# Kernel tuning notes

Hardware: AMD Instinct MI355X
Metric: run time of the kernel (lower is better)

The kernel has to match this reference:

```python
import jax, jax.numpy as jnp
import numpy as np

N_NODES = 100000
N_EDGES = 1600000
D_IN = 128
D_OUT = 128


def setup_inputs() -> dict:
    key = jax.random.key(0)
    k1, k2, k3 = jax.random.split(key, 3)
    input_matrix = jax.random.normal(k1, (N_NODES, D_IN), dtype=jnp.float32)
    adjacency_coo_matrix = jax.random.randint(k2, (2, N_EDGES), 0, N_NODES, dtype=jnp.int64)
    # xavier-uniform-like init for the projection weights
    limit = float(np.sqrt(6.0 / (D_IN + D_OUT)))
    W = jax.random.uniform(k3, (D_IN, D_OUT), minval=-limit, maxval=limit, dtype=jnp.float32)
    return {"input_matrix": input_matrix, "adjacency_coo_matrix": adjacency_coo_matrix, "W": W}


def reference(input_matrix, adjacency_coo_matrix, W):
    N = input_matrix.shape[0]
    # add self edges (i -> i) for every node
    self_idx = jnp.arange(N, dtype=adjacency_coo_matrix.dtype)
    src = jnp.concatenate([adjacency_coo_matrix[0], self_idx])  # segment ids (rows of output)
    nbr = jnp.concatenate([adjacency_coo_matrix[1], self_idx])  # gather indices
    # gather neighbor features: [E+N, d_in]
    neighbors = input_matrix[nbr]
    # scatter-mean over destination nodes
    summed = jax.ops.segment_sum(neighbors, src, num_segments=N)
    counts = jax.ops.segment_sum(jnp.ones((src.shape[0],), dtype=input_matrix.dtype), src, num_segments=N)
    mean = summed / counts[:, None]  # counts >= 1 thanks to self edges
    # linear projection
    return mean @ W
```

## Files before the change

kernel.cpp:

```cpp
#include <hip/hip_runtime.h>
#include <stdint.h>

#define DIM 128
#define SB 256

typedef unsigned short u16;
typedef unsigned int u32;
typedef __attribute__((ext_vector_type(8))) short short8;
typedef __attribute__((ext_vector_type(4))) float floatx4;
typedef __attribute__((ext_vector_type(4))) float nt_f32x4;
typedef __attribute__((ext_vector_type(4))) int i32x4;

__device__ __forceinline__ u16 f2bf(float f) {
    u32 u = __float_as_uint(f);
    if ((u & 0x7fffffffu) > 0x7f800000u) return (u16)0x7fc0;
    return (u16)((u + 0x7fffu + ((u >> 16) & 1u)) >> 16);
}

__global__ void __launch_bounds__(256) k_wprep(const float* __restrict__ W,
                                               u16* __restrict__ Wbf,
                                               u16* __restrict__ Yzero,
                                               int* __restrict__ cursor, int N) {
    int g = blockIdx.x * 256 + threadIdx.x;
    if (g < DIM * DIM) {
        int n = g >> 7, k = g & 127;
        Wbf[g] = f2bf(W[k * DIM + n]);
    }
    if (g < N) cursor[g] = 0;
    if (blockIdx.x == 0 && threadIdx.x < 32)
        ((ushort4*)Yzero)[threadIdx.x] = make_ushort4(0, 0, 0, 0);
}

__global__ void __launch_bounds__(512) k_fused(const float4* __restrict__ X4,
                                               const u16* __restrict__ Wbf,
                                               u16* __restrict__ Ybf,
                                               const int* __restrict__ adj,
                                               int* __restrict__ cursor,
                                               int* __restrict__ slots,
                                               int E, int N, int cap, int G, int T) {
    __shared__ __align__(16) u16 wt[DIM * 136];
    int b = blockIdx.x;
    long a0 = ((long)b * G) / T;
    long a1 = ((long)(b + 1) * G) / T;
    if (a1 > a0) {
        int gb = (int)a0;
        int t = threadIdx.x;
        for (int i = t; i < DIM * 16; i += 512) {
            int row = i >> 4, c8 = i & 15;
            *(short8*)&wt[row * 136 + c8 * 8] = *(const short8*)&Wbf[row * 128 + c8 * 8];
        }
        __syncthreads();
        int w = t >> 6, l = t & 63;
        int q = l >> 4, c = l & 15;
        int row0 = (gb * 8 + w) * 16;
        size_t mr = (size_t)min(row0 + c, N - 1) * 32;
        const nt_f32x4* Xnt = (const nt_f32x4*)X4;
        nt_f32x4 u[8];
        #pragma unroll
        for (int kt = 0; kt < 4; ++kt) {
            u[2 * kt]     = __builtin_nontemporal_load(&Xnt[mr + kt * 8 + q * 2]);
            u[2 * kt + 1] = __builtin_nontemporal_load(&Xnt[mr + kt * 8 + q * 2 + 1]);
        }
        floatx4 acc[8] = {};
        #pragma unroll
        for (int kt = 0; kt < 4; ++kt) {
            short8 a;
            nt_f32x4 u0 = u[2 * kt], u1 = u[2 * kt + 1];
            a[0] = (short)f2bf(u0.x); a[1] = (short)f2bf(u0.y);
            a[2] = (short)f2bf(u0.z); a[3] = (short)f2bf(u0.w);
            a[4] = (short)f2bf(u1.x); a[5] = (short)f2bf(u1.y);
            a[6] = (short)f2bf(u1.z); a[7] = (short)f2bf(u1.w);
            #pragma unroll
            for (int nt = 0; nt < 8; ++nt) {
                short8 bb = *(const short8*)&wt[(nt * 16 + c) * 136 + kt * 32 + q * 8];
                acc[nt] = __builtin_amdgcn_mfma_f32_16x16x32_bf16(a, bb, acc[nt], 0, 0, 0);
            }
        }
        #pragma unroll
        for (int r = 0; r < 4; ++r) {
            int orow = row0 + q * 4 + r;
            if (orow < N) {
                u16* yrow = Ybf + (size_t)orow * DIM;
                #pragma unroll
                for (int nt = 0; nt < 8; ++nt)
                    __builtin_nontemporal_store(f2bf(acc[nt][r]), &yrow[nt * 16 + c]);
            }
        }
    } else {
        int sid = b - (int)a1;
        int r = sid & 7;
        int sub = sid >> 3;
        int lo = N / 8 * r + min(r, N % 8);
        int hi = lo + N / 8 + (r < N % 8 ? 1 : 0);
        const i32x4* v4 = (const i32x4*)adj;
        int npair = E >> 3;
        int p = sub * 512 + threadIdx.x;
        if (p < npair) {
            i32x4 s0 = __builtin_nontemporal_load(&v4[2 * p]);
            i32x4 s1 = __builtin_nontemporal_load(&v4[2 * p + 1]);
            int e0 = p * 8;
            int nb[8];
            #pragma unroll
            for (int k = 0; k < 8; ++k)
                nb[k] = __builtin_nontemporal_load(&adj[E + e0 + k]);
            int ds[8] = {s0.x, s0.y, s0.z, s0.w, s1.x, s1.y, s1.z, s1.w};
            int cc[8];
            #pragma unroll
            for (int k = 0; k < 8; ++k) {
                bool hit = (ds[k] >= lo) & (ds[k] < hi);
                cc[k] = hit ? atomicAdd(&cursor[ds[k]], 1) : cap;
            }
            #pragma unroll
            for (int k = 0; k < 8; ++k) {
                if (cc[k] < cap)
                    slots[(size_t)ds[k] * cap + cc[k]] =
                        ((unsigned)nb[k] < (unsigned)N) ? nb[k] : 0;
            }
        }
        if (sub == 0) {
            int tail = E & 7;
            if (threadIdx.x < tail) {
                int e = (E & ~7) + threadIdx.x;
                int d = adj[e];
                if (d >= lo && d < hi) {
                    int nbv = adj[E + e];
                    int c = atomicAdd(&cursor[d], 1);
                    if (c < cap)
                        slots[(size_t)d * cap + c] =
                            ((unsigned)nbv < (unsigned)N) ? nbv : 0;
                }
            }
        }
    }
}

__device__ __forceinline__ void agg_core(const uint4* __restrict__ Yb4,
                                         const int* __restrict__ lst, int deg,
                                         int wid, int grp, int sl, int N,
                                         float4* __restrict__ out4) {
    float acc[8];
    {
        int id0 = (grp == 0) ? wid : N;
        uint4 v = Yb4[(size_t)id0 * 16 + sl];
        u32 c0[4] = {v.x, v.y, v.z, v.w};
        #pragma unroll
        for (int k2 = 0; k2 < 4; ++k2) {
            acc[2 * k2]     = __uint_as_float(c0[k2] << 16);
            acc[2 * k2 + 1] = __uint_as_float(c0[k2] & 0xffff0000u);
        }
    }
    for (int base = 0; base < deg; base += 32) {
        int id[8];
        #pragma unroll
        for (int qi = 0; qi < 8; ++qi) {
            int ee = base + qi * 4 + grp;
            int t = __builtin_nontemporal_load(&lst[ee]);
            id[qi] = (ee < deg) ? t : N;
        }
        uint4 v[8];
        #pragma unroll
        for (int qi = 0; qi < 8; ++qi)
            v[qi] = Yb4[(size_t)id[qi] * 16 + sl];
        #pragma unroll
        for (int qi = 0; qi < 8; ++qi) {
            u32 c0[4] = {v[qi].x, v[qi].y, v[qi].z, v[qi].w};
            #pragma unroll
            for (int k2 = 0; k2 < 4; ++k2) {
                acc[2 * k2]     += __uint_as_float(c0[k2] << 16);
                acc[2 * k2 + 1] += __uint_as_float(c0[k2] & 0xffff0000u);
            }
        }
    }
    #pragma unroll
    for (int j = 0; j < 8; ++j) {
        acc[j] += __shfl_xor(acc[j], 16);
        acc[j] += __shfl_xor(acc[j], 32);
    }
    float inv = 1.0f / (float)(deg + 1);
    if (grp < 2) {
        nt_f32x4 o;
        o.x = acc[grp * 4 + 0] * inv; o.y = acc[grp * 4 + 1] * inv;
        o.z = acc[grp * 4 + 2] * inv; o.w = acc[grp * 4 + 3] * inv;
        __builtin_nontemporal_store(o, (nt_f32x4*)&out4[(size_t)wid * 32 + sl * 2 + grp]);
    }
}

__global__ void __launch_bounds__(256) k_agg_cap(const uint4* __restrict__ Yb4,
                                                 const int* __restrict__ cnt,
                                                 const int* __restrict__ slots,
                                                 float4* __restrict__ out4, int N, int cap) {
    int wid = (blockIdx.x * 256 + threadIdx.x) >> 6;
    int lane = threadIdx.x & 63;
    if (wid >= N) return;
    int deg = min(cnt[wid], cap);
    agg_core(Yb4, slots + (size_t)wid * cap, deg, wid, lane >> 4, lane & 15, N, out4);
}

__global__ void __launch_bounds__(256) k_agg_off(const uint4* __restrict__ Yb4,
                                                 const int* __restrict__ offsets,
                                                 const int* __restrict__ sorted_nbr,
                                                 float4* __restrict__ out4, int N) {
    int wid = (blockIdx.x * 256 + threadIdx.x) >> 6;
    int lane = threadIdx.x & 63;
    if (wid >= N) return;
    int beg = offsets[wid], end = offsets[wid + 1];
    agg_core(Yb4, sorted_nbr + beg, end - beg, wid, lane >> 4, lane & 15, N, out4);
}

__global__ void __launch_bounds__(256) k_hist(const int* __restrict__ adj,
                                              int* __restrict__ counts, int E, int N) {
    int r = blockIdx.x & 7;
    int sub = blockIdx.x >> 3;
    int nsub = gridDim.x >> 3;
    int lo = N / 8 * r + min(r, N % 8);
    int hi = lo + N / 8 + (r < N % 8 ? 1 : 0);
    for (int e = sub * 256 + threadIdx.x; e < E; e += nsub * 256) {
        int d = adj[e];
        if (d >= lo && d < hi) atomicAdd(&counts[d], 1);
    }
}

__global__ void __launch_bounds__(SB) k_bsum(const int* __restrict__ counts,
                                             int* __restrict__ partials, int N) {
    __shared__ int lds[SB];
    int t = threadIdx.x;
    int i = blockIdx.x * SB + t;
    lds[t] = (i < N) ? counts[i] : 0;
    __syncthreads();
    for (int off = SB / 2; off > 0; off >>= 1) {
        if (t < off) lds[t] += lds[t + off];
        __syncthreads();
    }
    if (t == 0) partials[blockIdx.x] = lds[0];
}

__global__ void __launch_bounds__(1024) k_pscan(int* __restrict__ partials,
                                                int* __restrict__ offsets, int nb, int N) {
    __shared__ int lds[1024];
    int t = threadIdx.x;
    int v0 = (t < nb) ? partials[t] : 0;
    lds[t] = v0;
    __syncthreads();
    for (int off = 1; off < 1024; off <<= 1) {
        int v = (t >= off) ? lds[t - off] : 0;
        __syncthreads();
        lds[t] += v;
        __syncthreads();
    }
    if (t < nb) partials[t] = lds[t] - v0;
    if (t == 1023) offsets[N] = lds[1023];
}

__global__ void __launch_bounds__(SB) k_scan_final(const int* __restrict__ counts_in,
                                                   const int* __restrict__ partials,
                                                   int* __restrict__ offsets,
                                                   int* __restrict__ cursor, int N) {
    __shared__ int lds[SB];
    int t = threadIdx.x;
    int i = blockIdx.x * SB + t;
    int c = (i < N) ? counts_in[i] : 0;
    lds[t] = c;
    __syncthreads();
    for (int off = 1; off < SB; off <<= 1) {
        int v = (t >= off) ? lds[t - off] : 0;
        __syncthreads();
        lds[t] += v;
        __syncthreads();
    }
    int excl = lds[t] - c + partials[blockIdx.x];
    if (i < N) {
        offsets[i] = excl;
        cursor[i] = excl;
    }
}

__global__ void __launch_bounds__(256) k_reorder(const int* __restrict__ adj,
                                                 int* __restrict__ cursor,
                                                 int* __restrict__ sorted_nbr, int E, int N) {
    int r = blockIdx.x & 7;
    int sub = blockIdx.x >> 3;
    int nsub = gridDim.x >> 3;
    int lo = N / 8 * r + min(r, N % 8);
    int hi = lo + N / 8 + (r < N % 8 ? 1 : 0);
    for (int e = sub * 256 + threadIdx.x; e < E; e += nsub * 256) {
        int d = adj[e];
        if (d < lo || d >= hi) continue;
        int nb = adj[E + e];
        int pos = atomicAdd(&cursor[d], 1);
        sorted_nbr[pos] = ((unsigned)nb < (unsigned)N) ? nb : 0;
    }
}

__global__ void __launch_bounds__(512) k_gemm_y(const float4* __restrict__ X4,
                                                const u16* __restrict__ Wbf,
                                                u16* __restrict__ Ybf, int N) {
    __shared__ __align__(16) u16 wt[DIM * 136];
    int t = threadIdx.x;
    for (int i = t; i < DIM * 16; i += 512) {
        int row = i >> 4, c8 = i & 15;
        *(short8*)&wt[row * 136 + c8 * 8] = *(const short8*)&Wbf[row * 128 + c8 * 8];
    }
    __syncthreads();
    int w = t >> 6, l = t & 63;
    int q = l >> 4, c = l & 15;
    int row0 = (blockIdx.x * 8 + w) * 16;
    size_t mr = (size_t)min(row0 + c, N - 1) * 32;
    float4 u[8];
    #pragma unroll
    for (int kt = 0; kt < 4; ++kt) {
        u[2 * kt]     = X4[mr + kt * 8 + q * 2];
        u[2 * kt + 1] = X4[mr + kt * 8 + q * 2 + 1];
    }
    floatx4 acc[8] = {};
    #pragma unroll
    for (int kt = 0; kt < 4; ++kt) {
        short8 a;
        float4 u0 = u[2 * kt], u1 = u[2 * kt + 1];
        a[0] = (short)f2bf(u0.x); a[1] = (short)f2bf(u0.y);
        a[2] = (short)f2bf(u0.z); a[3] = (short)f2bf(u0.w);
        a[4] = (short)f2bf(u1.x); a[5] = (short)f2bf(u1.y);
        a[6] = (short)f2bf(u1.z); a[7] = (short)f2bf(u1.w);
        #pragma unroll
        for (int nt = 0; nt < 8; ++nt) {
            short8 bb = *(const short8*)&wt[(nt * 16 + c) * 136 + kt * 32 + q * 8];
            acc[nt] = __builtin_amdgcn_mfma_f32_16x16x32_bf16(a, bb, acc[nt], 0, 0, 0);
        }
    }
    #pragma unroll
    for (int r = 0; r < 4; ++r) {
        int orow = row0 + q * 4 + r;
        if (orow < N) {
            u16* yrow = Ybf + (size_t)orow * DIM;
            #pragma unroll
            for (int nt = 0; nt < 8; ++nt)
                yrow[nt * 16 + c] = f2bf(acc[nt][r]);
        }
    }
}

extern "C" void kernel_launch(void* const* d_in, const int* in_sizes, int n_in,
                              void* d_out, int out_size, void* d_ws, size_t ws_size,
                              hipStream_t stream) {
    int N = in_sizes[0] / DIM;
    int E = in_sizes[1] / 2;
    const float* X = (const float*)d_in[0];
    const int* adj = (const int*)d_in[1];
    const float* W = (const float*)d_in[2];
    float* out = (float*)d_out;

    int G = (N + 127) / 128;
    int npair = E >> 3;
    int S = 8 * ((npair + 511) / 512);
    int T = G + S;

    int wprep_blocks = (N + 255) / 256;

    size_t cur_b  = (size_t)N * 4;
    size_t y_b    = ((size_t)N + 1) * DIM * 2;
    size_t wbf_b  = (size_t)DIM * DIM * 2;

    int cap = 0;
    if (ws_size >= cur_b + (size_t)N * 64 * 4 + y_b + wbf_b) cap = 64;
    else if (ws_size >= cur_b + (size_t)N * 48 * 4 + y_b + wbf_b) cap = 48;

    if (cap) {
        int* cursor = (int*)d_ws;
        int* slots  = cursor + N;
        u16* Ybf    = (u16*)(slots + (size_t)N * cap);
        u16* Wbf    = Ybf + ((size_t)N + 1) * DIM;

        k_wprep<<<wprep_blocks, 256, 0, stream>>>(W, Wbf, Ybf + (size_t)N * DIM, cursor, N);
        k_fused<<<T, 512, 0, stream>>>((const float4*)X, Wbf, Ybf, adj, cursor, slots,
                                       E, N, cap, G, T);
        k_agg_cap<<<(N + 3) / 4, 256, 0, stream>>>((const uint4*)Ybf, cursor, slots,
                                                   (float4*)out, N, cap);
    } else {
        int nb = (N + SB - 1) / SB;
        int* cursor     = (int*)d_ws;
        int* offsets    = cursor + N;
        int* sorted_nbr = offsets + (N + 1);
        int* partials   = sorted_nbr + E;
        u16* Ybf        = (u16*)(partials + 512);
        u16* Wbf        = Ybf + ((size_t)N + 1) * DIM;

        k_wprep<<<wprep_blocks, 256, 0, stream>>>(W, Wbf, Ybf + (size_t)N * DIM, cursor, N);
        k_gemm_y<<<G, 512, 0, stream>>>((const float4*)X, Wbf, Ybf, N);
        k_hist<<<1024, 256, 0, stream>>>(adj, cursor, E, N);
        k_bsum<<<nb, SB, 0, stream>>>(cursor, partials, N);
        k_pscan<<<1, 1024, 0, stream>>>(partials, offsets, nb, N);
        k_scan_final<<<nb, SB, 0, stream>>>(cursor, partials, offsets, cursor, N);
        k_reorder<<<1024, 256, 0, stream>>>(adj, cursor, sorted_nbr, E, N);
        k_agg_off<<<(N + 3) / 4, 256, 0, stream>>>((const uint4*)Ybf, offsets, sorted_nbr,
                                                   (float4*)out, N);
    }
}
```

Before: 249.9 us.

## Map fused GEMM and bucket work per XCD and drop nontemporal hints

Block indices are now split by b&7 so each of the eight interleaved block groups (matching the round-robin XCD dispatch on MI355X) handles its own GEMM row tiles and its own destination-range bucket fill. This keeps each slot-range's atomics and writes, and its share of Y tiles, within one XCD's L2. Nontemporal loads and stores are also replaced with ordinary accesses so Y and the adjacency data can stay in cache for the later aggregation. The risk is less even load balance and extra cache pressure from the streamed X reads.

```diff
diff --git a/kernel.cpp b/kernel.cpp
--- a/kernel.cpp
+++ b/kernel.cpp
@@ -9,7 +9,6 @@
 typedef __attribute__((ext_vector_type(8))) short short8;
 typedef __attribute__((ext_vector_type(4))) float floatx4;
 typedef __attribute__((ext_vector_type(4))) float nt_f32x4;
-typedef __attribute__((ext_vector_type(4))) int i32x4;
 
 __device__ __forceinline__ u16 f2bf(float f) {
     u32 u = __float_as_uint(f);
@@ -37,13 +36,20 @@
                                                const int* __restrict__ adj,
                                                int* __restrict__ cursor,
                                                int* __restrict__ slots,
-                                               int E, int N, int cap, int G, int T) {
+                                               int E, int N, int cap, int G) {
     __shared__ __align__(16) u16 wt[DIM * 136];
     int b = blockIdx.x;
-    long a0 = ((long)b * G) / T;
-    long a1 = ((long)(b + 1) * G) / T;
+    int x = b & 7;
+    int u = b >> 3;
+    int npair = E >> 3;
+    int Sx = (npair + 511) / 512;
+    int Gx = (G + 7 - x) / 8;
+    int Ux = Gx + Sx;
+    if (u >= Ux) return;
+    long a0 = ((long)u * Gx) / Ux;
+    long a1 = ((long)(u + 1) * Gx) / Ux;
     if (a1 > a0) {
-        int gb = (int)a0;
+        int gb = (int)a0 * 8 + x;
         int t = threadIdx.x;
         for (int i = t; i < DIM * 16; i += 512) {
             int row = i >> 4, c8 = i & 15;
@@ -54,18 +60,17 @@
         int q = l >> 4, c = l & 15;
         int row0 = (gb * 8 + w) * 16;
         size_t mr = (size_t)min(row0 + c, N - 1) * 32;
-        const nt_f32x4* Xnt = (const nt_f32x4*)X4;
-        nt_f32x4 u[8];
+        float4 uv[8];
         #pragma unroll
         for (int kt = 0; kt < 4; ++kt) {
-            u[2 * kt]     = __builtin_nontemporal_load(&Xnt[mr + kt * 8 + q * 2]);
-            u[2 * kt + 1] = __builtin_nontemporal_load(&Xnt[mr + kt * 8 + q * 2 + 1]);
+            uv[2 * kt]     = X4[mr + kt * 8 + q * 2];
+            uv[2 * kt + 1] = X4[mr + kt * 8 + q * 2 + 1];
         }
         floatx4 acc[8] = {};
         #pragma unroll
         for (int kt = 0; kt < 4; ++kt) {
             short8 a;
-            nt_f32x4 u0 = u[2 * kt], u1 = u[2 * kt + 1];
+            float4 u0 = uv[2 * kt], u1 = uv[2 * kt + 1];
             a[0] = (short)f2bf(u0.x); a[1] = (short)f2bf(u0.y);
             a[2] = (short)f2bf(u0.z); a[3] = (short)f2bf(u0.w);
             a[4] = (short)f2bf(u1.x); a[5] = (short)f2bf(u1.y);
@@ -83,26 +88,23 @@
                 u16* yrow = Ybf + (size_t)orow * DIM;
                 #pragma unroll
                 for (int nt = 0; nt < 8; ++nt)
-                    __builtin_nontemporal_store(f2bf(acc[nt][r]), &yrow[nt * 16 + c]);
+                    yrow[nt * 16 + c] = f2bf(acc[nt][r]);
             }
         }
     } else {
-        int sid = b - (int)a1;
-        int r = sid & 7;
-        int sub = sid >> 3;
+        int sub = u - (int)a1;
+        int r = x;
         int lo = N / 8 * r + min(r, N % 8);
         int hi = lo + N / 8 + (r < N % 8 ? 1 : 0);
-        const i32x4* v4 = (const i32x4*)adj;
-        int npair = E >> 3;
+        const int4* v4 = (const int4*)adj;
         int p = sub * 512 + threadIdx.x;
         if (p < npair) {
-            i32x4 s0 = __builtin_nontemporal_load(&v4[2 * p]);
-            i32x4 s1 = __builtin_nontemporal_load(&v4[2 * p + 1]);
+            int4 s0 = v4[2 * p];
+            int4 s1 = v4[2 * p + 1];
             int e0 = p * 8;
             int nb[8];
             #pragma unroll
-            for (int k = 0; k < 8; ++k)
-                nb[k] = __builtin_nontemporal_load(&adj[E + e0 + k]);
+            for (int k = 0; k < 8; ++k) nb[k] = adj[E + e0 + k];
             int ds[8] = {s0.x, s0.y, s0.z, s0.w, s1.x, s1.y, s1.z, s1.w};
             int cc[8];
             #pragma unroll
@@ -350,8 +352,9 @@
 
     int G = (N + 127) / 128;
     int npair = E >> 3;
-    int S = 8 * ((npair + 511) / 512);
-    int T = G + S;
+    int Sx = (npair + 511) / 512;
+    int Gx0 = (G + 7) / 8;
+    int T = 8 * (Gx0 + Sx);
 
     int wprep_blocks = (N + 255) / 256;
 
@@ -371,7 +374,7 @@
 
         k_wprep<<<wprep_blocks, 256, 0, stream>>>(W, Wbf, Ybf + (size_t)N * DIM, cursor, N);
         k_fused<<<T, 512, 0, stream>>>((const float4*)X, Wbf, Ybf, adj, cursor, slots,
-                                       E, N, cap, G, T);
+                                       E, N, cap, G);
         k_agg_cap<<<(N + 3) / 4, 256, 0, stream>>>((const uint4*)Ybf, cursor, slots,
                                                    (float4*)out, N, cap);
     } else {
```

Result: faster. 232.3 us, median of 2 (-7.0%).
